# Optimization experiments

Hardware: AMD Instinct MI355X
Metric: run time of the kernel (lower is better)

## Reference

```python
import jax, jax.numpy as jnp
import numpy as np

B, S, M, D, H, F, E, K = 4, 1024, 1024, 1024, 16, 4096, 4, 2
DH = D // H
LB_COEF = 0.01
LN_EPS = 1e-5


def setup_inputs() -> dict:
    key = jax.random.key(0)
    ks = jax.random.split(key, 16)
    w = lambda k, shape: jax.random.normal(k, shape, jnp.float32) * 0.02
    return {
        "x": jax.random.normal(ks[0], (B, S, D), jnp.float32),
        "memory": jax.random.normal(ks[1], (B, M, D), jnp.float32),
        "sWq": w(ks[2], (D, D)), "sWk": w(ks[3], (D, D)),
        "sWv": w(ks[4], (D, D)), "sWo": w(ks[5], (D, D)),
        "cWq": w(ks[6], (D, D)), "cWk": w(ks[7], (D, D)),
        "cWv": w(ks[8], (D, D)), "cWo": w(ks[9], (D, D)),
        "Wg": w(ks[10], (E, D)),
        "W1": w(ks[11], (E, F, D)), "b1": jnp.zeros((E, F), jnp.float32),
        "W2": w(ks[12], (E, D, F)), "b2": jnp.zeros((E, D), jnp.float32),
        "ln1_g": jnp.ones((D,), jnp.float32), "ln1_b": jnp.zeros((D,), jnp.float32),
        "ln2_g": jnp.ones((D,), jnp.float32), "ln2_b": jnp.zeros((D,), jnp.float32),
        "ln3_g": jnp.ones((D,), jnp.float32), "ln3_b": jnp.zeros((D,), jnp.float32),
    }


def _ln(x, g, b):
    m = x.mean(-1, keepdims=True)
    v = ((x - m) ** 2).mean(-1, keepdims=True)
    return (x - m) * jax.lax.rsqrt(v + LN_EPS) * g + b


def _mha(q_in, k_in, v_in, Wq, Wk, Wv, Wo):
    # nn.Linear(bias=False): y = x @ W.T; split into heads [b, h, s, dh]
    def split(t):
        b, s, _ = t.shape
        return t.reshape(b, s, H, DH).transpose(0, 2, 1, 3)
    Q = split(q_in @ Wq.T)
    Kh = split(k_in @ Wk.T)
    V = split(v_in @ Wv.T)
    scores = jnp.einsum('bhqd,bhkd->bhqk', Q, Kh) / jnp.sqrt(jnp.float32(DH))
    attn = jax.nn.softmax(scores, axis=-1)  # dropout is identity in eval
    out = jnp.einsum('bhqk,bhkd->bhqd', attn, V)
    b, _, s, _ = out.shape
    out = out.transpose(0, 2, 1, 3).reshape(b, s, D)
    return out @ Wo.T


def _moe(h, Wg, W1, b1, W2, b2):
    gate_logits = h @ Wg.T                      # [B, S, E]
    gate_probs = jax.nn.softmax(gate_logits, -1)
    topk_logits, topk_idx = jax.lax.top_k(gate_logits, K)
    topk_w = jax.nn.softmax(topk_logits, -1)    # [B, S, K]
    # dense all-experts FFN (faithful to source): [B, S, E, F] hidden
    hid = jax.nn.gelu(jnp.einsum('bsd,efd->bsef', h, W1) + b1, approximate=False)
    eo = jnp.einsum('bsef,edf->bsed', hid, W2) + b2   # [B, S, E, D]
    sel = jnp.take_along_axis(eo, topk_idx[..., None], axis=2)  # [B, S, K, D]
    out = (sel * topk_w[..., None]).sum(axis=2)
    one_hot = jax.nn.one_hot(topk_idx, E, dtype=gate_probs.dtype)  # [B, S, K, E]
    load = one_hot.sum(axis=2).mean(axis=(0, 1))   # [E]
    imp = gate_probs.mean(axis=(0, 1))             # [E]
    aux = LB_COEF * (E * jnp.sum(load * imp))
    return out, aux


def reference(x, memory, sWq, sWk, sWv, sWo, cWq, cWk, cWv, cWo,
              Wg, W1, b1, W2, b2,
              ln1_g, ln1_b, ln2_g, ln2_b, ln3_g, ln3_b):
    h = _ln(x, ln1_g, ln1_b)
    x = x + _mha(h, h, h, sWq, sWk, sWv, sWo)
    h = _ln(x, ln2_g, ln2_b)
    x = x + _mha(h, memory, memory, cWq, cWk, cWv, cWo)
    h = _ln(x, ln3_g, ln3_b)
    ffn_out, aux = _moe(h, Wg, W1, b1, W2, b2)
    return (x + ffn_out, aux)
```

## Files before the change

kernel.cpp:

```cpp
#include <hip/hip_runtime.h>
#include <math.h>
#include <stdint.h>

typedef unsigned short u16;
typedef _Float16 f16;
typedef __attribute__((ext_vector_type(8))) _Float16 f16x8;
typedef __attribute__((ext_vector_type(8))) short s16x8;
typedef __attribute__((ext_vector_type(4))) float f32x4;
typedef __attribute__((ext_vector_type(4))) unsigned short u16x4;

#define DEV static __device__ __forceinline__

#define MFMA16(a, b, c) __builtin_amdgcn_mfma_f32_16x16x32_f16((a), (b), (c), 0, 0, 0)

DEV void split2(float v, u16& hi, u16& lo) {
  f16 h = (f16)v;
  f16 l = (f16)(v - (float)h);
  hi = __builtin_bit_cast(u16, h);
  lo = __builtin_bit_cast(u16, l);
}
DEV u16 f2h(float v) { f16 h = (f16)v; return __builtin_bit_cast(u16, h); }
DEV float h2f(u16 u) { f16 h = __builtin_bit_cast(f16, u); return (float)h; }

DEV void gload16(const void* gp, const void* lp) {
  typedef const __attribute__((address_space(1))) unsigned GU;
  typedef __attribute__((address_space(3))) unsigned LU;
  GU* g = (GU*)(uintptr_t)gp;
  LU* l = (LU*)(unsigned)(uintptr_t)lp;
  __builtin_amdgcn_global_load_lds(g, l, 16, 0, 0);
}

DEV int swzP(int q) { return ((q & 3) << 4) ^ (((q >> 2) & 3) << 5); }

enum { EPI3_SPLIT = 0, EPI3_RESID = 1 };

template <int EPI>
__global__ __launch_bounds__(512, 4)
void gemm3(const u16* __restrict__ Ah, const u16* __restrict__ Al,
           const u16* __restrict__ Bh, const u16* __restrict__ Bl,
           int N, int K, int ldC,
           u16* __restrict__ outh, u16* __restrict__ outl,
           float* __restrict__ outf, const float* __restrict__ resid)
{
  __shared__ alignas(16) u16 sAh[128 * 32], sAl[128 * 32];
  __shared__ alignas(16) u16 sBh[128 * 32], sBl[128 * 32];
  const int tid = threadIdx.x;
  const int wave = tid >> 6, lane = tid & 63;
  const int wr = wave >> 2, wc = wave & 3;
  const int li = lane & 15, g = lane >> 4;
  const long row0 = (long)blockIdx.y * 128;
  const int col0 = blockIdx.x * 128;

  const int srow = tid >> 2;
  const int scol = (tid & 3) * 8;
  const long arow = (row0 + srow) * (long)K + scol;
  const long brow = ((long)col0 + srow) * (long)K + scol;
  const u16 *gAh = Ah + arow, *gAl = Al + arow;
  const u16 *gBh = Bh + brow, *gBl = Bl + brow;
  const int wbase = wave * 512;

  const f32x4 fz = {0.f, 0.f, 0.f, 0.f};
  f32x4 acc[4][2];
#pragma unroll
  for (int m = 0; m < 4; m++)
#pragma unroll
    for (int n = 0; n < 2; n++) acc[m][n] = fz;

  const int aoff = (wr * 64 + li) * 32 + g * 8;
  const int boff = (wc * 32 + li) * 32 + g * 8;

  for (int k0 = 0; k0 < K; k0 += 32) {
    gload16(gAh + k0, sAh + wbase);
    gload16(gAl + k0, sAl + wbase);
    gload16(gBh + k0, sBh + wbase);
    gload16(gBl + k0, sBl + wbase);
    __syncthreads();
    f16x8 ah[4], al4[4], bh[2], bl4[2];
#pragma unroll
    for (int m = 0; m < 4; m++) {
      ah[m] = *(const f16x8*)(sAh + aoff + m * 512);
      al4[m] = *(const f16x8*)(sAl + aoff + m * 512);
    }
#pragma unroll
    for (int n = 0; n < 2; n++) {
      bh[n] = *(const f16x8*)(sBh + boff + n * 512);
      bl4[n] = *(const f16x8*)(sBl + boff + n * 512);
    }
#pragma unroll
    for (int m = 0; m < 4; m++)
#pragma unroll
      for (int n = 0; n < 2; n++) {
        f32x4 t = acc[m][n];
        t = MFMA16(al4[m], bh[n], t);
        t = MFMA16(ah[m], bl4[n], t);
        t = MFMA16(ah[m], bh[n], t);
        acc[m][n] = t;
      }
    __syncthreads();
  }

#pragma unroll
  for (int m = 0; m < 4; m++)
#pragma unroll
    for (int n = 0; n < 2; n++) {
      const int col = col0 + wc * 32 + n * 16 + li;
#pragma unroll
      for (int r = 0; r < 4; r++) {
        const long row = row0 + wr * 64 + m * 16 + g * 4 + r;
        const long idx = row * ldC + col;
        const float v = acc[m][n][r];
        if constexpr (EPI == EPI3_SPLIT) {
          u16 hi, lo; split2(v, hi, lo);
          outh[idx] = hi; outl[idx] = lo;
        } else {
          outf[idx] = resid[idx] + v;
        }
      }
    }
}

__global__ __launch_bounds__(256)
void vtrans(const u16* __restrict__ Vh, const u16* __restrict__ Vl,
            u16* __restrict__ Th, u16* __restrict__ Tl)
{
  __shared__ u16 t0[64][80];
  __shared__ u16 t1[64][80];
  const int kb = blockIdx.x, h = blockIdx.y, b = blockIdx.z;
  const int tid = threadIdx.x;
  const int r = tid >> 2;
  const int c = tid & 3;
  const long srow = ((long)b * 1024 + kb * 64 + r) * 3072 + h * 64;
  s16x8 a0 = *(const s16x8*)(Vh + srow + c * 8);
  s16x8 a1 = *(const s16x8*)(Vh + srow + c * 8 + 32);
  s16x8 b0 = *(const s16x8*)(Vl + srow + c * 8);
  s16x8 b1 = *(const s16x8*)(Vl + srow + c * 8 + 32);
#pragma unroll
  for (int j = 0; j < 8; j++) {
    t0[c * 8 + j][r]      = (u16)(short)a0[j];
    t0[c * 8 + 32 + j][r] = (u16)(short)a1[j];
    t1[c * 8 + j][r]      = (u16)(short)b0[j];
    t1[c * 8 + 32 + j][r] = (u16)(short)b1[j];
  }
  __syncthreads();
  const int dh = tid >> 2;
  const long drow = ((long)(b * 16 + h) * 64 + dh) * 1024 + kb * 64;
  s16x8 o0, o1;
#pragma unroll
  for (int j = 0; j < 8; j++) {
    o0[j] = (short)t0[dh][c * 8 + j];
    o1[j] = (short)t0[dh][c * 8 + 32 + j];
  }
  *(s16x8*)(Th + drow + c * 8) = o0;
  *(s16x8*)(Th + drow + c * 8 + 32) = o1;
#pragma unroll
  for (int j = 0; j < 8; j++) {
    o0[j] = (short)t1[dh][c * 8 + j];
    o1[j] = (short)t1[dh][c * 8 + 32 + j];
  }
  *(s16x8*)(Tl + drow + c * 8) = o0;
  *(s16x8*)(Tl + drow + c * 8 + 32) = o1;
}

__global__ __launch_bounds__(512, 4)
void attn3(const u16* __restrict__ Qh, const u16* __restrict__ Ql,
           const u16* __restrict__ Kbh, const u16* __restrict__ Kbl,
           const u16* __restrict__ Vth, const u16* __restrict__ Vtl,
           u16* __restrict__ AOh, u16* __restrict__ AOl)
{
  __shared__ alignas(16) u16 lKh[64 * 64], lKl[64 * 64];
  __shared__ alignas(16) u16 lVh[64 * 64], lVl[64 * 64];
  __shared__ alignas(16) u16 lPh[8 * 16 * 64], lPl[8 * 16 * 64];
  const int tid = threadIdx.x;
  const int wave = tid >> 6, lane = tid & 63;
  const int li = lane & 15, g = lane >> 4;
  const int qt = blockIdx.x, h = blockIdx.y, b = blockIdx.z;
  const int bh = b * 16 + h;
  const int LD = 3072;

  const long qrow0 = (long)b * 1024 + qt * 128 + wave * 16;
  f16x8 qfh[2], qfl[2];
#pragma unroll
  for (int kk = 0; kk < 2; kk++) {
    const long qoff = (qrow0 + li) * LD + h * 64 + kk * 32 + g * 8;
    qfh[kk] = *(const f16x8*)(Qh + qoff);
    qfl[kk] = *(const f16x8*)(Ql + qoff);
  }

  const f32x4 fz = {0.f, 0.f, 0.f, 0.f};
  float m_run[4], l_run[4];
  f32x4 oacc[4];
#pragma unroll
  for (int r = 0; r < 4; r++) { m_run[r] = -INFINITY; l_run[r] = 0.f; }
#pragma unroll
  for (int d = 0; d < 4; d++) oacc[d] = fz;

  char* cKh = (char*)lKh; char* cKl = (char*)lKl;
  char* cVh = (char*)lVh; char* cVl = (char*)lVl;
  char* cPh = (char*)lPh + wave * 2048;
  char* cPl = (char*)lPl + wave * 2048;

  const int kr = tid >> 3;
  const int kce = (tid & 7) * 8;
  const u16* kbase_h = Kbh + ((long)b * 1024 + kr) * LD + h * 64 + kce;
  const u16* kbase_l = Kbl + ((long)b * 1024 + kr) * LD + h * 64 + kce;
  const u16* vbase_h = Vth + ((long)bh * 64 + kr) * 1024 + kce;
  const u16* vbase_l = Vtl + ((long)bh * 64 + kr) * 1024 + kce;
  const int sdst = kr * 128 + ((kce * 2) ^ ((kr & 7) << 4));

  s16x8 rkh, rkl, rvh, rvl;
#define LOADT(t)                                                   \
  {                                                                \
    const long ko = (long)(t) * 64 * LD;                           \
    const int vo = (t) * 64;                                       \
    rkh = *(const s16x8*)(kbase_h + ko);                           \
    rkl = *(const s16x8*)(kbase_l + ko);                           \
    rvh = *(const s16x8*)(vbase_h + vo);                           \
    rvl = *(const s16x8*)(vbase_l + vo);                           \
  }

  LOADT(0);

  for (int t = 0; t < 16; ++t) {
    __syncthreads();
    *(s16x8*)(cKh + sdst) = rkh;
    *(s16x8*)(cKl + sdst) = rkl;
    *(s16x8*)(cVh + sdst) = rvh;
    *(s16x8*)(cVl + sdst) = rvl;
    if (t < 15) LOADT(t + 1);
    __syncthreads();

    f32x4 s[4];
#pragma unroll
    for (int cb = 0; cb < 4; cb++) {
      f32x4 tt = fz;
      const int key = cb * 16 + li;
#pragma unroll
      for (int kk = 0; kk < 2; kk++) {
        const int off = key * 128 + (((kk * 32 + g * 8) * 2) ^ ((key & 7) << 4));
        f16x8 fh = *(const f16x8*)(cKh + off);
        f16x8 fl = *(const f16x8*)(cKl + off);
        tt = MFMA16(qfl[kk], fh, tt);
        tt = MFMA16(qfh[kk], fl, tt);
        tt = MFMA16(qfh[kk], fh, tt);
      }
      s[cb] = tt;
    }
#pragma unroll
    for (int cb = 0; cb < 4; cb++)
#pragma unroll
      for (int r = 0; r < 4; r++) s[cb][r] *= 0.125f;

#pragma unroll
    for (int r = 0; r < 4; r++) {
      float mx = fmaxf(fmaxf(s[0][r], s[1][r]), fmaxf(s[2][r], s[3][r]));
      mx = fmaxf(mx, __shfl_xor(mx, 1));
      mx = fmaxf(mx, __shfl_xor(mx, 2));
      mx = fmaxf(mx, __shfl_xor(mx, 4));
      mx = fmaxf(mx, __shfl_xor(mx, 8));
      float mnew = fmaxf(m_run[r], mx);
      float sc = __expf(m_run[r] - mnew);
      m_run[r] = mnew;
      float ls = 0.f;
#pragma unroll
      for (int cb = 0; cb < 4; cb++) {
        float p = __expf(s[cb][r] - mnew);
        s[cb][r] = p;
        ls += p;
      }
      ls += __shfl_xor(ls, 1);
      ls += __shfl_xor(ls, 2);
      ls += __shfl_xor(ls, 4);
      ls += __shfl_xor(ls, 8);
      l_run[r] = l_run[r] * sc + ls;
#pragma unroll
      for (int d = 0; d < 4; d++) oacc[d][r] *= sc;
    }

#pragma unroll
    for (int cb = 0; cb < 4; cb++)
#pragma unroll
      for (int r = 0; r < 4; r++) {
        const int q = g * 4 + r;
        const int key = cb * 16 + li;
        const int off = q * 128 + ((key * 2) ^ swzP(q));
        u16 hi, lo; split2(s[cb][r], hi, lo);
        *(u16*)(cPh + off) = hi;
        *(u16*)(cPl + off) = lo;
      }

#pragma unroll
    for (int kk = 0; kk < 2; kk++) {
      const int kbyte = (kk * 32 + g * 8) * 2;
      const int poff = li * 128 + (kbyte ^ swzP(li));
      f16x8 pfh = *(const f16x8*)(cPh + poff);
      f16x8 pfl = *(const f16x8*)(cPl + poff);
#pragma unroll
      for (int d = 0; d < 4; d++) {
        const int dh = d * 16 + li;
        const int voff = dh * 128 + (kbyte ^ ((dh & 7) << 4));
        f16x8 vfh = *(const f16x8*)(cVh + voff);
        f16x8 vfl = *(const f16x8*)(cVl + voff);
        f32x4 tacc = oacc[d];
        tacc = MFMA16(pfl, vfh, tacc);
        tacc = MFMA16(pfh, vfl, tacc);
        tacc = MFMA16(pfh, vfh, tacc);
        oacc[d] = tacc;
      }
    }
  }
#undef LOADT

#pragma unroll
  for (int d = 0; d < 4; d++)
#pragma unroll
    for (int r = 0; r < 4; r++) {
      const long row = qrow0 + g * 4 + r;
      const int col = h * 64 + d * 16 + li;
      u16 hi, lo; split2(oacc[d][r] / l_run[r], hi, lo);
      AOh[row * 1024 + col] = hi;
      AOl[row * 1024 + col] = lo;
    }
}

template <bool GATE>
__global__ __launch_bounds__(256)
void ln_kernel(const float* __restrict__ x, const float* __restrict__ gam,
               const float* __restrict__ bet, u16* __restrict__ hh,
               u16* __restrict__ hl,
               const float* __restrict__ Wg, float* __restrict__ glog)
{
  const int row = blockIdx.x;
  const int tid = threadIdx.x;
  const int wave = tid >> 6, lane = tid & 63;
  const float* xr = x + (long)row * 1024;
  float4 v = *(const float4*)(xr + tid * 4);
  float s = v.x + v.y + v.z + v.w;
  float s2 = v.x * v.x + v.y * v.y + v.z * v.z + v.w * v.w;
#pragma unroll
  for (int m = 1; m < 64; m <<= 1) { s += __shfl_xor(s, m); s2 += __shfl_xor(s2, m); }
  __shared__ float red1[4], red2[4];
  if (lane == 0) { red1[wave] = s; red2[wave] = s2; }
  __syncthreads();
  float S = red1[0] + red1[1] + red1[2] + red1[3];
  float S2 = red2[0] + red2[1] + red2[2] + red2[3];
  float mean = S * (1.f / 1024.f);
  float var = S2 * (1.f / 1024.f) - mean * mean;
  float rstd = 1.f / sqrtf(var + 1e-5f);
  const int c = tid * 4;
  float hv[4];
  hv[0] = (v.x - mean) * rstd * gam[c + 0] + bet[c + 0];
  hv[1] = (v.y - mean) * rstd * gam[c + 1] + bet[c + 1];
  hv[2] = (v.z - mean) * rstd * gam[c + 2] + bet[c + 2];
  hv[3] = (v.w - mean) * rstd * gam[c + 3] + bet[c + 3];
  u16x4 oh, ol;
#pragma unroll
  for (int j = 0; j < 4; j++) {
    u16 hi, lo; split2(hv[j], hi, lo);
    oh[j] = hi; ol[j] = lo;
  }
  *(u16x4*)(hh + (long)row * 1024 + c) = oh;
  *(u16x4*)(hl + (long)row * 1024 + c) = ol;

  if constexpr (GATE) {
    float pe[4];
#pragma unroll
    for (int e = 0; e < 4; e++) {
      const float* wr_ = Wg + e * 1024 + c;
      pe[e] = hv[0] * wr_[0] + hv[1] * wr_[1] + hv[2] * wr_[2] + hv[3] * wr_[3];
    }
#pragma unroll
    for (int e = 0; e < 4; e++)
#pragma unroll
      for (int m = 1; m < 64; m <<= 1) pe[e] += __shfl_xor(pe[e], m);
    __shared__ float gred[4][4];
    if (lane == 0) {
#pragma unroll
      for (int e = 0; e < 4; e++) gred[wave][e] = pe[e];
    }
    __syncthreads();
    if (tid < 4)
      glog[(long)row * 4 + tid] = gred[0][tid] + gred[1][tid] + gred[2][tid] + gred[3][tid];
  }
}

__global__ __launch_bounds__(256)
void route_kernel(const float* __restrict__ glog,
                  int* __restrict__ tlist, float* __restrict__ wrow,
                  int4* __restrict__ meta, float2* __restrict__ wts,
                  int* __restrict__ scanMeta, float* __restrict__ outAux)
{
  const int tid = threadIdx.x;
  const int lane = tid & 63, wave = tid >> 6;
  __shared__ int scn[4][256];
  __shared__ int sTot[4];
  __shared__ int sBase[4];
  __shared__ float sred[4][8];

  for (int r = tid; r < 8704; r += 256) { tlist[r] = 0; wrow[r] = 0.f; }

  int myCnt[4] = {0, 0, 0, 0};
  float imp[4] = {0.f, 0.f, 0.f, 0.f}, ld[4] = {0.f, 0.f, 0.f, 0.f};
  unsigned char e1s[16], e2s[16];
  float w1s[16], w2s[16];
#pragma unroll 1
  for (int j = 0; j < 16; j++) {
    const int t = tid * 16 + j;
    float l[4];
#pragma unroll
    for (int e = 0; e < 4; e++) l[e] = glog[t * 4 + e];
    int e1 = 0; float bv = l[0];
#pragma unroll
    for (int e = 1; e < 4; e++) if (l[e] > bv) { bv = l[e]; e1 = e; }
    int e2 = -1; float bv2 = -INFINITY;
#pragma unroll
    for (int e = 0; e < 4; e++) if (e != e1 && l[e] > bv2) { bv2 = l[e]; e2 = e; }
    float wq = expf(bv2 - bv);
    float w1 = 1.f / (1.f + wq), w2 = wq / (1.f + wq);
    float ps = 0.f, pv[4];
#pragma unroll
    for (int e = 0; e < 4; e++) { pv[e] = expf(l[e] - bv); ps += pv[e]; }
    float inv = 1.f / ps;
#pragma unroll
    for (int e = 0; e < 4; e++) imp[e] += pv[e] * inv;
    ld[e1] += 1.f; ld[e2] += 1.f;
    myCnt[e1]++; myCnt[e2]++;
    e1s[j] = (unsigned char)e1; e2s[j] = (unsigned char)e2;
    w1s[j] = w1; w2s[j] = w2;
  }
#pragma unroll
  for (int e = 0; e < 4; e++) scn[e][tid] = myCnt[e];
  __syncthreads();

  if (wave < 4) {
    int carry = 0;
    for (int seg = 0; seg < 4; seg++) {
      int v = scn[wave][seg * 64 + lane];
      const int orig = v;
#pragma unroll
      for (int d = 1; d < 64; d <<= 1) { int o = __shfl_up(v, d); if (lane >= d) v += o; }
      scn[wave][seg * 64 + lane] = carry + v - orig;
      carry += __shfl(v, 63);
    }
    if (lane == 0) sTot[wave] = carry;
  }
  __syncthreads();

  if (tid == 0) {
    int base = 0;
    for (int e = 0; e < 4; e++) {
      const int c = sTot[e];
      const int cap = (c + 127) & ~127;
      sBase[e] = base;
      const int t0 = base >> 7, t1 = (base + cap) >> 7;
      for (int i = t0; i < t1; i++) scanMeta[1 + i] = e;
      base += cap;
    }
    scanMeta[0] = base >> 7;
  }
  __syncthreads();

  int off[4];
#pragma unroll
  for (int e = 0; e < 4; e++) off[e] = sBase[e] + scn[e][tid];
#pragma unroll 1
  for (int j = 0; j < 16; j++) {
    const int t = tid * 16 + j;
    const int e1 = e1s[j], e2 = e2s[j];
    const int p1 = off[e1]++;
    const int p2 = off[e2]++;
    tlist[p1] = t; wrow[p1] = w1s[j];
    tlist[p2] = t; wrow[p2] = w2s[j];
    int4 m; m.x = p1; m.y = p2; m.z = e1; m.w = e2;
    meta[t] = m;
    float2 w; w.x = w1s[j]; w.y = w2s[j];
    wts[t] = w;
  }

#pragma unroll
  for (int e = 0; e < 4; e++) {
#pragma unroll
    for (int d = 1; d < 64; d <<= 1) {
      imp[e] += __shfl_xor(imp[e], d);
      ld[e] += __shfl_xor(ld[e], d);
    }
  }
  if (lane == 0) {
#pragma unroll
    for (int e = 0; e < 4; e++) { sred[wave][e] = imp[e]; sred[wave][4 + e] = ld[e]; }
  }
  __syncthreads();
  if (tid == 0) {
    float a = 0.f;
    for (int e = 0; e < 4; e++) {
      float im = sred[0][e] + sred[1][e] + sred[2][e] + sred[3][e];
      float lo = sred[0][4 + e] + sred[1][4 + e] + sred[2][4 + e] + sred[3][4 + e];
      a += (lo * (1.f / 4096.f)) * (im * (1.f / 4096.f));
    }
    outAux[0] = 0.01f * 4.f * a;
  }
}

__global__ __launch_bounds__(256, 2)
void gemm_up(const u16* __restrict__ A, const u16* __restrict__ w1h,
             const float* __restrict__ b1, const int* __restrict__ tlist,
             const float* __restrict__ wrow, const int* __restrict__ scanMeta,
             u16* __restrict__ hid)
{
  const int L = blockIdx.x;
  const int gg = (L & 7) * 272 + (L >> 3);
  const int rt = gg >> 5, cc = gg & 31;
  if (rt >= scanMeta[0]) return;
  const int e = scanMeta[1 + rt];
  __shared__ alignas(16) u16 lA[128 * 32];
  __shared__ alignas(16) u16 lB[128 * 32];
  const int tid = threadIdx.x;
  const int wave = tid >> 6, lane = tid & 63;
  const int wr = wave >> 1, wc = wave & 1;
  const int li = lane & 15, g = lane >> 4;
  const int row0 = rt * 128;
  const int col0 = cc * 128;

  const int srow = lane >> 2;
  const int scol = (lane & 3) * 8;
  const int r1 = row0 + wave * 32 + srow;
  const long t1 = tlist[r1], t2 = tlist[r1 + 16];
  const u16* gA1 = A + t1 * 1024 + scol;
  const u16* gA2 = A + t2 * 1024 + scol;
  const u16* gB = w1h + (size_t)e * 4194304 +
                  ((size_t)(col0 + wave * 32 + srow)) * 1024 + scol;
  u16* lAw = lA + wave * 1024;
  u16* lBw = lB + wave * 1024;

  const f32x4 fz = {0.f, 0.f, 0.f, 0.f};
  f32x4 acc[4][4];
#pragma unroll
  for (int m = 0; m < 4; m++)
#pragma unroll
    for (int n = 0; n < 4; n++) acc[m][n] = fz;

  const int aoff = (wr * 64 + li) * 32 + g * 8;
  const int boff = (wc * 64 + li) * 32 + g * 8;

  for (int k0 = 0; k0 < 1024; k0 += 32) {
    gload16(gA1 + k0, lAw);
    gload16(gA2 + k0, lAw + 512);
    gload16(gB + k0, lBw);
    gload16(gB + k0 + 16 * 1024, lBw + 512);
    __syncthreads();
    f16x8 af[4], bfr[4];
#pragma unroll
    for (int m = 0; m < 4; m++) af[m] = *(const f16x8*)(lA + aoff + m * 512);
#pragma unroll
    for (int n = 0; n < 4; n++) bfr[n] = *(const f16x8*)(lB + boff + n * 512);
#pragma unroll
    for (int m = 0; m < 4; m++)
#pragma unroll
      for (int n = 0; n < 4; n++)
        acc[m][n] = MFMA16(af[m], bfr[n], acc[m][n]);
    __syncthreads();
  }

#pragma unroll
  for (int m = 0; m < 4; m++)
#pragma unroll
    for (int n = 0; n < 4; n++) {
      const int col = col0 + wc * 64 + n * 16 + li;
#pragma unroll
      for (int r = 0; r < 4; r++) {
        const int row = row0 + wr * 64 + m * 16 + g * 4 + r;
        const float coef = wrow[row];
        float tv = acc[m][n][r] + b1[e * 4096 + col];
        float ge = 0.5f * tv * (1.f + erff(tv * 0.7071067811865475f));
        hid[(size_t)row * 4096 + col] = f2h(coef * ge);
      }
    }
}

__global__ __launch_bounds__(512, 4)
void gemm_down(const u16* __restrict__ hid, const u16* __restrict__ w2h,
               const int* __restrict__ scanMeta, u16* __restrict__ part)
{
  const int L = blockIdx.x;
  const int gg = (L & 7) * 68 + (L >> 3);
  const int rt = gg >> 3, cc = gg & 7;
  if (rt >= scanMeta[0]) return;
  const int e = scanMeta[1 + rt];
  __shared__ alignas(16) u16 lA[128 * 32];
  __shared__ alignas(16) u16 lB[128 * 32];
  const int tid = threadIdx.x;
  const int wave = tid >> 6, lane = tid & 63;
  const int wr = wave >> 2, wc = wave & 3;
  const int li = lane & 15, g = lane >> 4;
  const int row0 = rt * 128;
  const int col0 = cc * 128;

  const int srow = tid >> 2;
  const int scol = (tid & 3) * 8;
  const u16* gA = hid + ((size_t)(row0 + srow)) * 4096 + scol;
  const u16* gB = w2h + (size_t)e * 4194304 +
                  ((size_t)(col0 + srow)) * 4096 + scol;
  const int wbase = wave * 512;

  const f32x4 fz = {0.f, 0.f, 0.f, 0.f};
  f32x4 acc[4][2];
#pragma unroll
  for (int m = 0; m < 4; m++)
#pragma unroll
    for (int n = 0; n < 2; n++) acc[m][n] = fz;

  const int aoff = (wr * 64 + li) * 32 + g * 8;
  const int boff = (wc * 32 + li) * 32 + g * 8;

  for (int k0 = 0; k0 < 4096; k0 += 32) {
    gload16(gA + k0, lA + wbase);
    gload16(gB + k0, lB + wbase);
    __syncthreads();
    f16x8 af[4], bfr[2];
#pragma unroll
    for (int m = 0; m < 4; m++) af[m] = *(const f16x8*)(lA + aoff + m * 512);
#pragma unroll
    for (int n = 0; n < 2; n++) bfr[n] = *(const f16x8*)(lB + boff + n * 512);
#pragma unroll
    for (int m = 0; m < 4; m++)
#pragma unroll
      for (int n = 0; n < 2; n++)
        acc[m][n] = MFMA16(af[m], bfr[n], acc[m][n]);
    __syncthreads();
  }

#pragma unroll
  for (int m = 0; m < 4; m++)
#pragma unroll
    for (int n = 0; n < 2; n++) {
      const int col = col0 + wc * 32 + n * 16 + li;
#pragma unroll
      for (int r = 0; r < 4; r++) {
        const int row = row0 + wr * 64 + m * 16 + g * 4 + r;
        part[(size_t)row * 1024 + col] = f2h(acc[m][n][r]);
      }
    }
}

__global__ __launch_bounds__(256)
void merge_kernel(const float* __restrict__ xw, const u16* __restrict__ part,
                  const int4* __restrict__ meta, const float2* __restrict__ wts,
                  const float* __restrict__ b2, float* __restrict__ out)
{
  const long i = ((long)blockIdx.x * 256 + threadIdx.x) * 4;
  const int row = (int)(i >> 10), col = (int)(i & 1023);
  const int4 m = meta[row];
  const float2 w = wts[row];
  float4 a = *(const float4*)(xw + i);
  u16x4 p1 = *(const u16x4*)(part + (size_t)m.x * 1024 + col);
  u16x4 p2 = *(const u16x4*)(part + (size_t)m.y * 1024 + col);
  const float* b2a = b2 + m.z * 1024 + col;
  const float* b2b = b2 + m.w * 1024 + col;
  float av[4] = {a.x, a.y, a.z, a.w};
  float4 o;
  float ov[4];
#pragma unroll
  for (int j = 0; j < 4; j++)
    ov[j] = av[j] + h2f(p1[j]) + h2f(p2[j]) + w.x * b2a[j] + w.y * b2b[j];
  o.x = ov[0]; o.y = ov[1]; o.z = ov[2]; o.w = ov[3];
  *(float4*)(out + i) = o;
}

__global__ __launch_bounds__(256)
void cvt_h(const float* __restrict__ src, u16* __restrict__ dst)
{
  const long i = ((long)blockIdx.x * 256 + threadIdx.x) * 4;
  float4 v = *(const float4*)(src + i);
  u16x4 o = {f2h(v.x), f2h(v.y), f2h(v.z), f2h(v.w)};
  *(u16x4*)(dst + i) = o;
}

__global__ __launch_bounds__(256)
void cvt_split(const float* __restrict__ src, u16* __restrict__ dh, u16* __restrict__ dl)
{
  const long i = ((long)blockIdx.x * 256 + threadIdx.x) * 4;
  float4 v = *(const float4*)(src + i);
  u16x4 oh, ol;
  float vv[4] = {v.x, v.y, v.z, v.w};
#pragma unroll
  for (int j = 0; j < 4; j++) { u16 a, b; split2(vv[j], a, b); oh[j] = a; ol[j] = b; }
  *(u16x4*)(dh + i) = oh;
  *(u16x4*)(dl + i) = ol;
}

struct Ptr8 { const float* p[8]; };

__global__ __launch_bounds__(256)
void cvt8_split(Ptr8 ps, u16* __restrict__ dh, u16* __restrict__ dl)
{
  const int w = blockIdx.y;
  const long i = ((long)blockIdx.x * 256 + threadIdx.x) * 4;
  float4 v = *(const float4*)(ps.p[w] + i);
  u16x4 oh, ol;
  float vv[4] = {v.x, v.y, v.z, v.w};
#pragma unroll
  for (int j = 0; j < 4; j++) { u16 a, b; split2(vv[j], a, b); oh[j] = a; ol[j] = b; }
  *(u16x4*)(dh + (long)w * 1048576 + i) = oh;
  *(u16x4*)(dl + (long)w * 1048576 + i) = ol;
}

extern "C" void kernel_launch(void* const* d_in, const int* in_sizes, int n_in,
                              void* d_out, int out_size, void* d_ws, size_t ws_size,
                              hipStream_t stream)
{
  const float* x    = (const float*)d_in[0];
  const float* mem  = (const float*)d_in[1];
  const float* sWq  = (const float*)d_in[2];
  const float* sWk  = (const float*)d_in[3];
  const float* sWv  = (const float*)d_in[4];
  const float* sWo  = (const float*)d_in[5];
  const float* cWq  = (const float*)d_in[6];
  const float* cWk  = (const float*)d_in[7];
  const float* cWv  = (const float*)d_in[8];
  const float* cWo  = (const float*)d_in[9];
  const float* Wg   = (const float*)d_in[10];
  const float* W1   = (const float*)d_in[11];
  const float* b1   = (const float*)d_in[12];
  const float* W2   = (const float*)d_in[13];
  const float* b2   = (const float*)d_in[14];
  const float* ln1g = (const float*)d_in[15];
  const float* ln1b = (const float*)d_in[16];
  const float* ln2g = (const float*)d_in[17];
  const float* ln2b = (const float*)d_in[18];
  const float* ln3g = (const float*)d_in[19];
  const float* ln3b = (const float*)d_in[20];
  float* out = (float*)d_out;
  (void)in_sizes; (void)n_in; (void)out_size; (void)ws_size;

  char* ws = (char*)d_ws;
  size_t off = 0;
  auto alloc = [&](size_t bytes) -> void* {
    void* p = ws + off; off += (bytes + 255) & ~(size_t)255; return p;
  };
  float* xw    = (float*)alloc((size_t)4096 * 1024 * 4);
  u16*   hh    = (u16*)  alloc((size_t)4096 * 1024 * 2);
  u16*   hl    = (u16*)  alloc((size_t)4096 * 1024 * 2);
  u16*   memh  = (u16*)  alloc((size_t)4096 * 1024 * 2);
  u16*   meml  = (u16*)  alloc((size_t)4096 * 1024 * 2);
  u16*   qkvh  = (u16*)  alloc((size_t)4096 * 3072 * 2);
  u16*   qkvl  = (u16*)  alloc((size_t)4096 * 3072 * 2);
  u16*   aoh   = (u16*)  alloc((size_t)4096 * 1024 * 2);
  u16*   aol   = (u16*)  alloc((size_t)4096 * 1024 * 2);
  u16*   aWh   = (u16*)  alloc((size_t)8 * 1024 * 1024 * 2);
  u16*   aWl   = (u16*)  alloc((size_t)8 * 1024 * 1024 * 2);
  u16*   w1h   = (u16*)  alloc((size_t)4 * 4096 * 1024 * 2);
  u16*   w2h   = (u16*)  alloc((size_t)4 * 4096 * 1024 * 2);
  float* glog  = (float*)alloc((size_t)4096 * 4 * 4);
  int*   tlist = (int*)  alloc((size_t)8704 * 4);
  float* wrow  = (float*)alloc((size_t)8704 * 4);
  int4*  meta  = (int4*) alloc((size_t)4096 * 16);
  float2* wts  = (float2*)alloc((size_t)4096 * 8);
  int*   scanM = (int*)  alloc((size_t)128 * 4);
  u16*   vth = hh;
  u16*   vtl = hl;
  u16*   hid = qkvh;
  u16*   part = (u16*)hh;

  Ptr8 p8;
  p8.p[0] = sWq; p8.p[1] = sWk; p8.p[2] = sWv; p8.p[3] = sWo;
  p8.p[4] = cWq; p8.p[5] = cWk; p8.p[6] = cWv; p8.p[7] = cWo;
  cvt8_split<<<dim3(1024, 8), 256, 0, stream>>>(p8, aWh, aWl);
  cvt_h<<<16384, 256, 0, stream>>>(W1, w1h);
  cvt_h<<<16384, 256, 0, stream>>>(W2, w2h);
  cvt_split<<<4096, 256, 0, stream>>>(mem, memh, meml);

  ln_kernel<false><<<4096, 256, 0, stream>>>(x, ln1g, ln1b, hh, hl, nullptr, nullptr);
  gemm3<EPI3_SPLIT><<<dim3(24, 32), 512, 0, stream>>>(hh, hl, aWh, aWl, 3072, 1024, 3072,
                                                      qkvh, qkvl, nullptr, nullptr);
  vtrans<<<dim3(16, 16, 4), 256, 0, stream>>>(qkvh + 2048, qkvl + 2048, vth, vtl);
  attn3<<<dim3(8, 16, 4), 512, 0, stream>>>(qkvh, qkvl, qkvh + 1024, qkvl + 1024,
                                            vth, vtl, aoh, aol);
  gemm3<EPI3_RESID><<<dim3(8, 32), 512, 0, stream>>>(aoh, aol, aWh + (size_t)3 * 1048576,
                                                     aWl + (size_t)3 * 1048576, 1024, 1024, 1024,
                                                     nullptr, nullptr, xw, x);

  ln_kernel<false><<<4096, 256, 0, stream>>>(xw, ln2g, ln2b, hh, hl, nullptr, nullptr);
  gemm3<EPI3_SPLIT><<<dim3(8, 32), 512, 0, stream>>>(hh, hl, aWh + (size_t)4 * 1048576,
                                                     aWl + (size_t)4 * 1048576, 1024, 1024, 3072,
                                                     qkvh, qkvl, nullptr, nullptr);
  gemm3<EPI3_SPLIT><<<dim3(16, 32), 512, 0, stream>>>(memh, meml, aWh + (size_t)5 * 1048576,
                                                      aWl + (size_t)5 * 1048576, 2048, 1024, 3072,
                                                      qkvh + 1024, qkvl + 1024, nullptr, nullptr);
  vtrans<<<dim3(16, 16, 4), 256, 0, stream>>>(qkvh + 2048, qkvl + 2048, vth, vtl);
  attn3<<<dim3(8, 16, 4), 512, 0, stream>>>(qkvh, qkvl, qkvh + 1024, qkvl + 1024,
                                            vth, vtl, aoh, aol);
  gemm3<EPI3_RESID><<<dim3(8, 32), 512, 0, stream>>>(aoh, aol, aWh + (size_t)7 * 1048576,
                                                     aWl + (size_t)7 * 1048576, 1024, 1024, 1024,
                                                     nullptr, nullptr, xw, xw);

  ln_kernel<true><<<4096, 256, 0, stream>>>(xw, ln3g, ln3b, hh, hl, Wg, glog);
  route_kernel<<<1, 256, 0, stream>>>(glog, tlist, wrow, meta, wts, scanM,
                                      out + (size_t)4096 * 1024);
  gemm_up<<<2176, 256, 0, stream>>>(hh, w1h, b1, tlist, wrow, scanM, hid);
  gemm_down<<<544, 512, 0, stream>>>(hid, w2h, scanM, part);
  merge_kernel<<<4096, 256, 0, stream>>>(xw, part, meta, wts, b2, out);
}
```

Before: 850.4 us.

## Double-buffer LDS tiles in split, up and down GEMM k-loops

```diff
diff --git a/kernel.cpp b/kernel.cpp
--- a/kernel.cpp
+++ b/kernel.cpp
@@ -42,8 +42,8 @@
            u16* __restrict__ outh, u16* __restrict__ outl,
            float* __restrict__ outf, const float* __restrict__ resid)
 {
-  __shared__ alignas(16) u16 sAh[128 * 32], sAl[128 * 32];
-  __shared__ alignas(16) u16 sBh[128 * 32], sBl[128 * 32];
+  __shared__ alignas(16) u16 sAh[2][128 * 32], sAl[2][128 * 32];
+  __shared__ alignas(16) u16 sBh[2][128 * 32], sBl[2][128 * 32];
   const int tid = threadIdx.x;
   const int wave = tid >> 6, lane = tid & 63;
   const int wr = wave >> 2, wc = wave & 3;
@@ -69,22 +69,31 @@
   const int aoff = (wr * 64 + li) * 32 + g * 8;
   const int boff = (wc * 32 + li) * 32 + g * 8;
 
-  for (int k0 = 0; k0 < K; k0 += 32) {
-    gload16(gAh + k0, sAh + wbase);
-    gload16(gAl + k0, sAl + wbase);
-    gload16(gBh + k0, sBh + wbase);
-    gload16(gBl + k0, sBl + wbase);
+  gload16(gAh, &sAh[0][wbase]);
+  gload16(gAl, &sAl[0][wbase]);
+  gload16(gBh, &sBh[0][wbase]);
+  gload16(gBl, &sBl[0][wbase]);
+
+  int cur = 0;
+  for (int k0 = 0; k0 < K; k0 += 32, cur ^= 1) {
     __syncthreads();
+    const int nxt = cur ^ 1;
+    if (k0 + 32 < K) {
+      gload16(gAh + k0 + 32, &sAh[nxt][wbase]);
+      gload16(gAl + k0 + 32, &sAl[nxt][wbase]);
+      gload16(gBh + k0 + 32, &sBh[nxt][wbase]);
+      gload16(gBl + k0 + 32, &sBl[nxt][wbase]);
+    }
     f16x8 ah[4], al4[4], bh[2], bl4[2];
 #pragma unroll
     for (int m = 0; m < 4; m++) {
-      ah[m] = *(const f16x8*)(sAh + aoff + m * 512);
-      al4[m] = *(const f16x8*)(sAl + aoff + m * 512);
+      ah[m] = *(const f16x8*)(&sAh[cur][aoff + m * 512]);
+      al4[m] = *(const f16x8*)(&sAl[cur][aoff + m * 512]);
     }
 #pragma unroll
     for (int n = 0; n < 2; n++) {
-      bh[n] = *(const f16x8*)(sBh + boff + n * 512);
-      bl4[n] = *(const f16x8*)(sBl + boff + n * 512);
+      bh[n] = *(const f16x8*)(&sBh[cur][boff + n * 512]);
+      bl4[n] = *(const f16x8*)(&sBl[cur][boff + n * 512]);
     }
 #pragma unroll
     for (int m = 0; m < 4; m++)
@@ -96,7 +105,6 @@
         t = MFMA16(ah[m], bh[n], t);
         acc[m][n] = t;
       }
-    __syncthreads();
   }
 
 #pragma unroll
@@ -511,8 +519,8 @@
   const int rt = gg >> 5, cc = gg & 31;
   if (rt >= scanMeta[0]) return;
   const int e = scanMeta[1 + rt];
-  __shared__ alignas(16) u16 lA[128 * 32];
-  __shared__ alignas(16) u16 lB[128 * 32];
+  __shared__ alignas(16) u16 lA[2][128 * 32];
+  __shared__ alignas(16) u16 lB[2][128 * 32];
   const int tid = threadIdx.x;
   const int wave = tid >> 6, lane = tid & 63;
   const int wr = wave >> 1, wc = wave & 1;
@@ -528,8 +536,7 @@
   const u16* gA2 = A + t2 * 1024 + scol;
   const u16* gB = w1h + (size_t)e * 4194304 +
                   ((size_t)(col0 + wave * 32 + srow)) * 1024 + scol;
-  u16* lAw = lA + wave * 1024;
-  u16* lBw = lB + wave * 1024;
+  const int wbase = wave * 1024;
 
   const f32x4 fz = {0.f, 0.f, 0.f, 0.f};
   f32x4 acc[4][4];
@@ -541,23 +548,31 @@
   const int aoff = (wr * 64 + li) * 32 + g * 8;
   const int boff = (wc * 64 + li) * 32 + g * 8;
 
-  for (int k0 = 0; k0 < 1024; k0 += 32) {
-    gload16(gA1 + k0, lAw);
-    gload16(gA2 + k0, lAw + 512);
-    gload16(gB + k0, lBw);
-    gload16(gB + k0 + 16 * 1024, lBw + 512);
+  gload16(gA1, &lA[0][wbase]);
+  gload16(gA2, &lA[0][wbase + 512]);
+  gload16(gB, &lB[0][wbase]);
+  gload16(gB + 16 * 1024, &lB[0][wbase + 512]);
+
+  int cur = 0;
+  for (int k0 = 0; k0 < 1024; k0 += 32, cur ^= 1) {
     __syncthreads();
+    const int nxt = cur ^ 1;
+    if (k0 + 32 < 1024) {
+      gload16(gA1 + k0 + 32, &lA[nxt][wbase]);
+      gload16(gA2 + k0 + 32, &lA[nxt][wbase + 512]);
+      gload16(gB + k0 + 32, &lB[nxt][wbase]);
+      gload16(gB + k0 + 32 + 16 * 1024, &lB[nxt][wbase + 512]);
+    }
     f16x8 af[4], bfr[4];
 #pragma unroll
-    for (int m = 0; m < 4; m++) af[m] = *(const f16x8*)(lA + aoff + m * 512);
-#pragma unroll
-    for (int n = 0; n < 4; n++) bfr[n] = *(const f16x8*)(lB + boff + n * 512);
+    for (int m = 0; m < 4; m++) af[m] = *(const f16x8*)(&lA[cur][aoff + m * 512]);
+#pragma unroll
+    for (int n = 0; n < 4; n++) bfr[n] = *(const f16x8*)(&lB[cur][boff + n * 512]);
 #pragma unroll
     for (int m = 0; m < 4; m++)
 #pragma unroll
       for (int n = 0; n < 4; n++)
         acc[m][n] = MFMA16(af[m], bfr[n], acc[m][n]);
-    __syncthreads();
   }
 
 #pragma unroll
@@ -585,8 +600,8 @@
   const int rt = gg >> 3, cc = gg & 7;
   if (rt >= scanMeta[0]) return;
   const int e = scanMeta[1 + rt];
-  __shared__ alignas(16) u16 lA[128 * 32];
-  __shared__ alignas(16) u16 lB[128 * 32];
+  __shared__ alignas(16) u16 lA[2][128 * 32];
+  __shared__ alignas(16) u16 lB[2][128 * 32];
   const int tid = threadIdx.x;
   const int wave = tid >> 6, lane = tid & 63;
   const int wr = wave >> 2, wc = wave & 3;
@@ -611,21 +626,27 @@
   const int aoff = (wr * 64 + li) * 32 + g * 8;
   const int boff = (wc * 32 + li) * 32 + g * 8;
 
-  for (int k0 = 0; k0 < 4096; k0 += 32) {
-    gload16(gA + k0, lA + wbase);
-    gload16(gB + k0, lB + wbase);
+  gload16(gA, &lA[0][wbase]);
+  gload16(gB, &lB[0][wbase]);
+
+  int cur = 0;
+  for (int k0 = 0; k0 < 4096; k0 += 32, cur ^= 1) {
     __syncthreads();
+    const int nxt = cur ^ 1;
+    if (k0 + 32 < 4096) {
+      gload16(gA + k0 + 32, &lA[nxt][wbase]);
+      gload16(gB + k0 + 32, &lB[nxt][wbase]);
+    }
     f16x8 af[4], bfr[2];
 #pragma unroll
-    for (int m = 0; m < 4; m++) af[m] = *(const f16x8*)(lA + aoff + m * 512);
-#pragma unroll
-    for (int n = 0; n < 2; n++) bfr[n] = *(const f16x8*)(lB + boff + n * 512);
+    for (int m = 0; m < 4; m++) af[m] = *(const f16x8*)(&lA[cur][aoff + m * 512]);
+#pragma unroll
+    for (int n = 0; n < 2; n++) bfr[n] = *(const f16x8*)(&lB[cur][boff + n * 512]);
 #pragma unroll
     for (int m = 0; m < 4; m++)
 #pragma unroll
       for (int n = 0; n < 2; n++)
         acc[m][n] = MFMA16(af[m], bfr[n], acc[m][n]);
-    __syncthreads();
   }
 
 #pragma unroll
```

Measured after the change: 791.8 us. 1.07x faster.
